# Optimization experiments

Measured on AMD Instinct MI355X. Metric: run time of the kernel, lower is better.

The kernel has to match this reference:

```python
import jax, jax.numpy as jnp
import numpy as np
from jax import lax

# ---- module hyperparams (match init_kwargs and mamba_ssm Mamba2 defaults) ----
D_MODEL = 768
D_STATE = 64
D_CONV = 4
EXPAND = 2
HEADDIM = 64  # Mamba2 default
D_INNER = EXPAND * D_MODEL          # 1536
NHEADS = D_INNER // HEADDIM         # 24
NGROUPS = 1
CONV_DIM = D_INNER + 2 * NGROUPS * D_STATE          # 1664
D_IN_PROJ = 2 * D_INNER + 2 * NGROUPS * D_STATE + NHEADS  # 3224
BSZ, SEQ = 2, 512
EPS = 1e-5


def setup_inputs() -> dict:
    key = jax.random.key(0)
    ks = jax.random.split(key, 12)
    def n(k, shape, s):
        return jax.random.normal(k, shape, jnp.float32) * s
    x = n(ks[0], (BSZ, SEQ, D_MODEL), 1.0)
    in_proj_w = n(ks[1], (D_IN_PROJ, D_MODEL), D_MODEL ** -0.5)
    conv_w = n(ks[2], (CONV_DIM, D_CONV), D_CONV ** -0.5)
    conv_b = jnp.zeros((CONV_DIM,), jnp.float32)
    # dt_bias = softplus^{-1}(dt) with dt log-uniform in [1e-3, 1e-1] (Mamba2 init)
    dt = jnp.exp(jax.random.uniform(ks[3], (NHEADS,), jnp.float32,
                                    minval=np.log(1e-3), maxval=np.log(1e-1)))
    dt_bias = dt + jnp.log(-jnp.expm1(-dt))
    A_log = jnp.log(jax.random.uniform(ks[4], (NHEADS,), jnp.float32, minval=1.0, maxval=16.0))
    D_param = jnp.ones((NHEADS,), jnp.float32)
    norm_w = jnp.ones((D_INNER,), jnp.float32)
    out_proj_w = n(ks[5], (D_MODEL, D_INNER), D_INNER ** -0.5)
    ln1_w = jnp.ones((D_MODEL,), jnp.float32); ln1_b = jnp.zeros((D_MODEL,), jnp.float32)
    ln2_w = jnp.ones((D_MODEL,), jnp.float32); ln2_b = jnp.zeros((D_MODEL,), jnp.float32)
    ff_w1 = n(ks[6], (4 * D_MODEL, D_MODEL), D_MODEL ** -0.5)
    ff_b1 = jnp.zeros((4 * D_MODEL,), jnp.float32)
    ff_w2 = n(ks[7], (D_MODEL, 4 * D_MODEL), (4 * D_MODEL) ** -0.5)
    ff_b2 = jnp.zeros((D_MODEL,), jnp.float32)
    return dict(x=x, in_proj_w=in_proj_w, conv_w=conv_w, conv_b=conv_b,
                dt_bias=dt_bias, A_log=A_log, D_param=D_param, norm_w=norm_w,
                out_proj_w=out_proj_w, ln1_w=ln1_w, ln1_b=ln1_b,
                ln2_w=ln2_w, ln2_b=ln2_b, ff_w1=ff_w1, ff_b1=ff_b1,
                ff_w2=ff_w2, ff_b2=ff_b2)


def layernorm(x, w, b):
    mu = jnp.mean(x, -1, keepdims=True)
    xc = x - mu
    var = jnp.mean(xc * xc, -1, keepdims=True)
    return xc * lax.rsqrt(var + EPS) * w + b


def mamba2(xn, in_proj_w, conv_w, conv_b, dt_bias, A_log, D_param, norm_w, out_proj_w):
    b, l, _ = xn.shape
    zxbcdt = xn @ in_proj_w.T  # [b, l, D_IN_PROJ]
    z = zxbcdt[..., :D_INNER]
    xBC = zxbcdt[..., D_INNER:D_INNER + CONV_DIM]
    dt = zxbcdt[..., D_INNER + CONV_DIM:]
    # causal depthwise conv over time on xBC
    xc = lax.conv_general_dilated(xBC.transpose(0, 2, 1), conv_w[:, None, :], (1,),
                                  [(D_CONV - 1, 0)], dimension_numbers=('NCH', 'OIH', 'NCH'),
                                  feature_group_count=CONV_DIM)
    xBC = jax.nn.silu((xc + conv_b[None, :, None]).transpose(0, 2, 1))
    xs = xBC[..., :D_INNER].reshape(b, l, NHEADS, HEADDIM)
    Bm = xBC[..., D_INNER:D_INNER + D_STATE]   # [b, l, n]  (ngroups=1)
    Cm = xBC[..., D_INNER + D_STATE:]          # [b, l, n]
    dt = jax.nn.softplus(dt + dt_bias)         # [b, l, h]
    dA = jnp.exp(dt * (-jnp.exp(A_log)))       # [b, l, h]
    dBx = jnp.einsum('blh,bln,blhp->blhpn', dt, Bm, xs)
    def step(h, inp):
        dA_t, dBx_t = inp                      # [b,h], [b,h,p,n]
        h = dA_t[:, :, None, None] * h + dBx_t
        return h, h
    _, hs = lax.scan(step, jnp.zeros((b, NHEADS, HEADDIM, D_STATE), xn.dtype),
                     (dA.transpose(1, 0, 2), dBx.transpose(1, 0, 2, 3, 4)))
    y = jnp.einsum('lbhpn,bln->blhp', hs, Cm) + D_param[None, None, :, None] * xs
    y = y.reshape(b, l, D_INNER) * jax.nn.silu(z)   # gated RMSNorm (norm_before_gate=False)
    y = y * lax.rsqrt(jnp.mean(y * y, -1, keepdims=True) + EPS) * norm_w
    return y @ out_proj_w.T


def reference(x, in_proj_w, conv_w, conv_b, dt_bias, A_log, D_param, norm_w,
              out_proj_w, ln1_w, ln1_b, ln2_w, ln2_b, ff_w1, ff_b1, ff_w2, ff_b2):
    residual = x
    xn = layernorm(x, ln1_w, ln1_b)
    mp = (in_proj_w, conv_w, conv_b, dt_bias, A_log, D_param, norm_w, out_proj_w)
    out_f = mamba2(xn, *mp)
    out_b = jnp.flip(mamba2(jnp.flip(xn, 1), *mp), 1)
    m = layernorm(out_f + out_b, ln2_w, ln2_b)
    ff = jax.nn.gelu(m @ ff_w1.T + ff_b1, approximate=False) @ ff_w2.T + ff_b2
    return ff + residual
```

## Files before the change

### kernel.cpp

```cpp
#include <hip/hip_runtime.h>
#include <hip/hip_bf16.h>
#include <math.h>

#define SEQ     512
#define BSZ     2
#define ROWS    (BSZ*SEQ)
#define DMODEL  768
#define DINNER  1536
#define DSTATE  64
#define NHEADS  24
#define HEADDIM 64
#define CONVDIM 1664
#define DINPROJ 3224
#define DFF     3072
#define EPSF    1e-5f

typedef __attribute__((ext_vector_type(8))) short s16x8;
typedef __attribute__((ext_vector_type(4))) float f32x4;

__device__ __forceinline__ float b2f(const __hip_bfloat16 v){ return __bfloat162float(v); }
__device__ __forceinline__ __hip_bfloat16 f2b(float v){ return __float2bfloat16(v); }
__device__ __forceinline__ ushort f2bu(float v){
  union { __hip_bfloat16 b; ushort u; } c; c.b = __float2bfloat16(v); return c.u;
}
__device__ __forceinline__ float u2f(ushort u){ return __uint_as_float(((uint)u) << 16); }

__device__ __forceinline__ void gload16(const void* g, void* l){
  __builtin_amdgcn_global_load_lds((__attribute__((address_space(1))) const void*)g,
                                   (__attribute__((address_space(3))) void*)l, 16, 0, 0);
}

__device__ __forceinline__ float block_sum256(float v, float* sh){
  #pragma unroll
  for (int off = 32; off > 0; off >>= 1) v += __shfl_down(v, off, 64);
  int w = threadIdx.x >> 6;
  if ((threadIdx.x & 63) == 0) sh[w] = v;
  __syncthreads();
  float t = sh[0] + sh[1] + sh[2] + sh[3];
  __syncthreads();
  return t;
}

__global__ __launch_bounds__(256) void zerof_kernel(float* out, int n){
  int i = blockIdx.x*256 + threadIdx.x;
  if (i < n) out[i] = 0.f;
}

__global__ __launch_bounds__(256) void w2ball_kernel(const float* __restrict__ w0,
    const float* __restrict__ w1, const float* __restrict__ w2,
    const float* __restrict__ w3, ushort* __restrict__ o,
    int n0, int n1, int n2, int n3)
{
  int i = (blockIdx.x*256 + threadIdx.x) << 2;
  int total = n0 + n1 + n2 + n3;
  if (i >= total) return;
  const float* s; int off;
  if      (i < n0)          { s = w0; off = i; }
  else if (i < n0+n1)       { s = w1; off = i - n0; }
  else if (i < n0+n1+n2)    { s = w2; off = i - n0 - n1; }
  else                      { s = w3; off = i - n0 - n1 - n2; }
  float4 f = *(const float4*)(s + off);
  ushort4 u = make_ushort4(f2bu(f.x), f2bu(f.y), f2bu(f.z), f2bu(f.w));
  *(ushort4*)(o + i) = u;
}

__global__ __launch_bounds__(256) void ln_kernel(const float* __restrict__ in,
    const float* __restrict__ w, const float* __restrict__ b,
    __hip_bfloat16* __restrict__ out)
{
  __shared__ float sh[4];
  const int row = blockIdx.x;
  const float* xr = in + (size_t)row * DMODEL;
  float v[3]; float s = 0.f;
  #pragma unroll
  for (int i = 0; i < 3; i++){ int c = threadIdx.x + i*256; v[i] = xr[c]; s += v[i]; }
  s = block_sum256(s, sh);
  float mu = s * (1.f/DMODEL);
  float s2 = 0.f;
  #pragma unroll
  for (int i = 0; i < 3; i++){ float d = v[i]-mu; s2 += d*d; }
  s2 = block_sum256(s2, sh);
  float rs = rsqrtf(s2*(1.f/DMODEL) + EPSF);
  #pragma unroll
  for (int i = 0; i < 3; i++){
    int c = threadIdx.x + i*256;
    out[(size_t)row*DMODEL + c] = f2b((v[i]-mu)*rs*w[c] + b[c]);
  }
}

__device__ __forceinline__ s16x8 ld_frag(const ushort* p){
  union { ushort4 h[2]; s16x8 v; } u;
  u.h[0] = *(const ushort4*)(p);
  u.h[1] = *(const ushort4*)(p + 4);
  return u.v;
}

template<typename CTy, int KS, int EPI>
__global__ __launch_bounds__(256) void gemm_bb64(const __hip_bfloat16* __restrict__ A_,
    const __hip_bfloat16* __restrict__ B_, CTy* __restrict__ C,
    const float* __restrict__ bias, int M, int N, int K)
{
  __shared__ __align__(16) ushort As[2][64][64];
  __shared__ __align__(16) ushort Bs[2][64][64];
  const int tid  = threadIdx.x;
  const int lane = tid & 63, wave = tid >> 6;
  const int wr = wave >> 1, wc = wave & 1;
  const int n0 = blockIdx.x * 64, m0 = blockIdx.y * 64;
  const int Kc   = K / KS;
  const int kbeg = blockIdx.z * Kc;
  const int srw  = lane >> 3;
  const int scol = (((lane & 7) ^ srw) << 3);
  const int l15  = lane & 15;
  const int r7   = l15 & 7;
  const int c0   = lane >> 4;

  const ushort* Au = (const ushort*)A_;
  const ushort* Bu = (const ushort*)B_;

  f32x4 acc[2][2] = {};

  auto stage = [&](int bf, int k0){
    #pragma unroll
    for (int q = 0; q < 2; q++){
      int row = q*32 + wave*8 + srw;
      gload16(Au + (size_t)(m0 + row)*K + kbeg + k0 + scol, &As[bf][q*32 + wave*8][0]);
      int nr = n0 + row; if (nr > N-1) nr = N-1;
      gload16(Bu + (size_t)nr*K + kbeg + k0 + scol, &Bs[bf][q*32 + wave*8][0]);
    }
  };

  stage(0, 0);
  __syncthreads();
  int cur = 0;
  for (int k0 = 0; k0 < Kc; k0 += 64){
    if (k0 + 64 < Kc) stage(cur ^ 1, k0 + 64);
    #pragma unroll
    for (int t = 0; t < 2; t++){
      const int fc = (((t*4 + c0) ^ r7) << 3);
      s16x8 a0 = ld_frag(&As[cur][wr*32      + l15][fc]);
      s16x8 a1 = ld_frag(&As[cur][wr*32 + 16 + l15][fc]);
      s16x8 b0 = ld_frag(&Bs[cur][wc*32      + l15][fc]);
      s16x8 b1 = ld_frag(&Bs[cur][wc*32 + 16 + l15][fc]);
      acc[0][0] = __builtin_amdgcn_mfma_f32_16x16x32_bf16(a0, b0, acc[0][0], 0, 0, 0);
      acc[0][1] = __builtin_amdgcn_mfma_f32_16x16x32_bf16(a0, b1, acc[0][1], 0, 0, 0);
      acc[1][0] = __builtin_amdgcn_mfma_f32_16x16x32_bf16(a1, b0, acc[1][0], 0, 0, 0);
      acc[1][1] = __builtin_amdgcn_mfma_f32_16x16x32_bf16(a1, b1, acc[1][1], 0, 0, 0);
    }
    __syncthreads();
    cur ^= 1;
  }

  CTy* Cz = C + (size_t)blockIdx.z * M * N;
  const int crow = (lane >> 4) * 4;
  #pragma unroll
  for (int i = 0; i < 2; i++){
    #pragma unroll
    for (int j = 0; j < 2; j++){
      int col = n0 + wc*32 + j*16 + l15;
      if (col < N){
        #pragma unroll
        for (int q = 0; q < 4; q++){
          int rowg = m0 + wr*32 + i*16 + crow + q;
          if constexpr (EPI == 1){
            float v = acc[i][j][q] + bias[col];
            Cz[(size_t)rowg*N + col] = (CTy)f2b(0.5f * v * (1.f + erff(v * 0.70710678118654752f)));
          } else if constexpr (sizeof(CTy) == 4){
            Cz[(size_t)rowg*N + col] = acc[i][j][q];
          } else {
            Cz[(size_t)rowg*N + col] = (CTy)f2b(acc[i][j][q]);
          }
        }
      }
    }
  }
}

template<typename CTy>
__global__ __launch_bounds__(256) void gemm_mfma(const __hip_bfloat16* __restrict__ A,
    const float* __restrict__ B, CTy* __restrict__ C, int M, int N, int K)
{
  __shared__ __align__(16) ushort As[64][72];
  __shared__ __align__(16) ushort Bs[64][72];
  const int tid  = threadIdx.x;
  const int lane = tid & 63, wave = tid >> 6;
  const int wr = wave >> 1, wc = wave & 1;
  const int n0 = blockIdx.x * 64, m0 = blockIdx.y * 64;
  const int sr = tid >> 2;
  const int sc = (tid & 3) * 16;
  const int l15 = lane & 15, lk = (lane >> 4) * 8;

  f32x4 acc[2][2] = {};

  const ushort* Au = (const ushort*)A;
  int nr = n0 + sr; if (nr > N-1) nr = N-1;

  for (int k0 = 0; k0 < K; k0 += 64){
    const ushort* ag = Au + (size_t)(m0 + sr)*K + (k0 + sc);
    ushort4 a0 = *(const ushort4*)(ag);
    ushort4 a1 = *(const ushort4*)(ag + 4);
    ushort4 a2 = *(const ushort4*)(ag + 8);
    ushort4 a3 = *(const ushort4*)(ag + 12);
    const float* bg = B + (size_t)nr*K + (k0 + sc);
    float4 f0 = *(const float4*)(bg);
    float4 f1 = *(const float4*)(bg + 4);
    float4 f2 = *(const float4*)(bg + 8);
    float4 f3 = *(const float4*)(bg + 12);
    ushort4 b0 = make_ushort4(f2bu(f0.x), f2bu(f0.y), f2bu(f0.z), f2bu(f0.w));
    ushort4 b1 = make_ushort4(f2bu(f1.x), f2bu(f1.y), f2bu(f1.z), f2bu(f1.w));
    ushort4 b2 = make_ushort4(f2bu(f2.x), f2bu(f2.y), f2bu(f2.z), f2bu(f2.w));
    ushort4 b3 = make_ushort4(f2bu(f3.x), f2bu(f3.y), f2bu(f3.z), f2bu(f3.w));

    __syncthreads();
    *(ushort4*)&As[sr][sc +  0] = a0;
    *(ushort4*)&As[sr][sc +  4] = a1;
    *(ushort4*)&As[sr][sc +  8] = a2;
    *(ushort4*)&As[sr][sc + 12] = a3;
    *(ushort4*)&Bs[sr][sc +  0] = b0;
    *(ushort4*)&Bs[sr][sc +  4] = b1;
    *(ushort4*)&Bs[sr][sc +  8] = b2;
    *(ushort4*)&Bs[sr][sc + 12] = b3;
    __syncthreads();

    #pragma unroll
    for (int kk = 0; kk < 64; kk += 32){
      s16x8 af0 = ld_frag(&As[wr*32      + l15][kk + lk]);
      s16x8 af1 = ld_frag(&As[wr*32 + 16 + l15][kk + lk]);
      s16x8 bf0 = ld_frag(&Bs[wc*32      + l15][kk + lk]);
      s16x8 bf1 = ld_frag(&Bs[wc*32 + 16 + l15][kk + lk]);
      acc[0][0] = __builtin_amdgcn_mfma_f32_16x16x32_bf16(af0, bf0, acc[0][0], 0, 0, 0);
      acc[0][1] = __builtin_amdgcn_mfma_f32_16x16x32_bf16(af0, bf1, acc[0][1], 0, 0, 0);
      acc[1][0] = __builtin_amdgcn_mfma_f32_16x16x32_bf16(af1, bf0, acc[1][0], 0, 0, 0);
      acc[1][1] = __builtin_amdgcn_mfma_f32_16x16x32_bf16(af1, bf1, acc[1][1], 0, 0, 0);
    }
  }

  const int crow = (lane >> 4) * 4;
  #pragma unroll
  for (int i = 0; i < 2; i++){
    #pragma unroll
    for (int j = 0; j < 2; j++){
      int col = n0 + wc*32 + j*16 + l15;
      if (col < N){
        #pragma unroll
        for (int q = 0; q < 4; q++){
          int rowg = m0 + wr*32 + i*16 + crow + q;
          if constexpr (sizeof(CTy) == 4) C[(size_t)rowg*N + col] = acc[i][j][q];
          else                            C[(size_t)rowg*N + col] = (CTy)f2b(acc[i][j][q]);
        }
      }
    }
  }
}

__global__ __launch_bounds__(256) void convdt_kernel(const __hip_bfloat16* __restrict__ zx,
    const float* __restrict__ cw, const float* __restrict__ cb,
    const float* __restrict__ dt_bias, const float* __restrict__ A_log,
    __hip_bfloat16* __restrict__ xconv, float* __restrict__ dtb, float* __restrict__ dab)
{
  const int tt = blockIdx.x, b = blockIdx.y, dir = blockIdx.z;
  const int c8 = threadIdx.x * 8;
  if (c8 < CONVDIM){
    size_t rowoff[4]; bool ok[4];
    #pragma unroll
    for (int k = 0; k < 4; k++){
      int s = tt - 3 + k;
      ok[k] = (s >= 0);
      int ss = ok[k] ? s : 0;
      int phys = dir ? (SEQ-1-ss) : ss;
      rowoff[k] = ((size_t)(b*SEQ + phys))*DINPROJ + DINNER + c8;
    }
    float acc[8];
    {
      float4 cb0 = *(const float4*)(cb + c8);
      float4 cb1 = *(const float4*)(cb + c8 + 4);
      acc[0]=cb0.x; acc[1]=cb0.y; acc[2]=cb0.z; acc[3]=cb0.w;
      acc[4]=cb1.x; acc[5]=cb1.y; acc[6]=cb1.z; acc[7]=cb1.w;
    }
    float wv[8][4];
    #pragma unroll
    for (int j = 0; j < 8; j++){
      float4 w4 = *(const float4*)(cw + (size_t)(c8 + j)*4);
      wv[j][0]=w4.x; wv[j][1]=w4.y; wv[j][2]=w4.z; wv[j][3]=w4.w;
    }
    const ushort* zu = (const ushort*)zx;
    #pragma unroll
    for (int k = 0; k < 4; k++){
      if (ok[k]){
        ushort4 v0 = *(const ushort4*)(zu + rowoff[k]);
        ushort4 v1 = *(const ushort4*)(zu + rowoff[k] + 4);
        acc[0] = fmaf(wv[0][k], u2f(v0.x), acc[0]);
        acc[1] = fmaf(wv[1][k], u2f(v0.y), acc[1]);
        acc[2] = fmaf(wv[2][k], u2f(v0.z), acc[2]);
        acc[3] = fmaf(wv[3][k], u2f(v0.w), acc[3]);
        acc[4] = fmaf(wv[4][k], u2f(v1.x), acc[4]);
        acc[5] = fmaf(wv[5][k], u2f(v1.y), acc[5]);
        acc[6] = fmaf(wv[6][k], u2f(v1.z), acc[6]);
        acc[7] = fmaf(wv[7][k], u2f(v1.w), acc[7]);
      }
    }
    ushort* outr = (ushort*)xconv + ((size_t)((dir*BSZ + b)*SEQ + tt))*CONVDIM + c8;
    ushort o[8];
    #pragma unroll
    for (int j = 0; j < 8; j++){
      float s = acc[j] / (1.f + expf(-acc[j]));
      o[j] = f2bu(s);
    }
    *(ushort4*)(outr)     = make_ushort4(o[0],o[1],o[2],o[3]);
    *(ushort4*)(outr + 4) = make_ushort4(o[4],o[5],o[6],o[7]);
  }
  if (dir == 0 && threadIdx.x < NHEADS){
    int h = threadIdx.x;
    size_t r = (size_t)b*SEQ + tt;
    float raw = b2f(zx[r*DINPROJ + (DINNER + CONVDIM) + h]) + dt_bias[h];
    float sp  = fmaxf(raw, 0.f) + log1pf(expf(-fabsf(raw)));
    dtb[r*NHEADS + h] = sp;
    dab[r*NHEADS + h] = expf(-sp * expf(A_log[h]));
  }
}

#define CT 16

__global__ __launch_bounds__(256) void scan_pass1(const __hip_bfloat16* __restrict__ xconv,
    const float* __restrict__ dtb, const float* __restrict__ dab,
    float* __restrict__ stateBuf, int CL)
{
  const int c = blockIdx.x, h = blockIdx.y, z = blockIdx.z;
  const int b = z & 1, dir = z >> 1;
  const int tid = threadIdx.x, lane = tid & 63, wave = tid >> 6, nb = wave * 16;
  __shared__ __align__(16) float Bc[CT][64], Xc[CT][64];
  __shared__ float dAc[CT], dtc[CT];
  float hreg[16];
  #pragma unroll
  for (int j = 0; j < 16; j++) hreg[j] = 0.f;
  const size_t dirbase = (size_t)z * SEQ;
  const int cstart = c * CL;

  const int ttl = tid >> 4, c4 = (tid & 15) << 2;

  for (int c0 = cstart; c0 < cstart + CL; c0 += CT){
    {
      const ushort* rowp = (const ushort*)xconv + (dirbase + c0 + ttl)*(size_t)CONVDIM;
      ushort4 bv = *(const ushort4*)(rowp + DINNER + c4);
      ushort4 xv = *(const ushort4*)(rowp + h*HEADDIM + c4);
      Bc[ttl][c4+0] = u2f(bv.x); Bc[ttl][c4+1] = u2f(bv.y);
      Bc[ttl][c4+2] = u2f(bv.z); Bc[ttl][c4+3] = u2f(bv.w);
      Xc[ttl][c4+0] = u2f(xv.x); Xc[ttl][c4+1] = u2f(xv.y);
      Xc[ttl][c4+2] = u2f(xv.z); Xc[ttl][c4+3] = u2f(xv.w);
    }
    if (tid < CT){
      int phys = dir ? (SEQ-1 - (c0 + tid)) : (c0 + tid);
      size_t r = (size_t)b*SEQ + phys;
      dAc[tid] = dab[r*NHEADS + h];
      dtc[tid] = dtb[r*NHEADS + h];
    }
    __syncthreads();

    #pragma unroll 4
    for (int tt = 0; tt < CT; tt++){
      float dA = dAc[tt];
      float dtx = dtc[tt] * Xc[tt][lane];
      const float4* Bq = (const float4*)&Bc[tt][nb];
      float4 B0 = Bq[0], B1 = Bq[1], B2 = Bq[2], B3 = Bq[3];
      hreg[ 0]=fmaf(dA,hreg[ 0],dtx*B0.x); hreg[ 1]=fmaf(dA,hreg[ 1],dtx*B0.y);
      hreg[ 2]=fmaf(dA,hreg[ 2],dtx*B0.z); hreg[ 3]=fmaf(dA,hreg[ 3],dtx*B0.w);
      hreg[ 4]=fmaf(dA,hreg[ 4],dtx*B1.x); hreg[ 5]=fmaf(dA,hreg[ 5],dtx*B1.y);
      hreg[ 6]=fmaf(dA,hreg[ 6],dtx*B1.z); hreg[ 7]=fmaf(dA,hreg[ 7],dtx*B1.w);
      hreg[ 8]=fmaf(dA,hreg[ 8],dtx*B2.x); hreg[ 9]=fmaf(dA,hreg[ 9],dtx*B2.y);
      hreg[10]=fmaf(dA,hreg[10],dtx*B2.z); hreg[11]=fmaf(dA,hreg[11],dtx*B2.w);
      hreg[12]=fmaf(dA,hreg[12],dtx*B3.x); hreg[13]=fmaf(dA,hreg[13],dtx*B3.y);
      hreg[14]=fmaf(dA,hreg[14],dtx*B3.z); hreg[15]=fmaf(dA,hreg[15],dtx*B3.w);
    }
    __syncthreads();
  }

  float* sp = stateBuf + (((size_t)c*4 + z)*NHEADS + h)*4096 + (size_t)lane*64 + nb;
  *(float4*)(sp +  0) = make_float4(hreg[ 0],hreg[ 1],hreg[ 2],hreg[ 3]);
  *(float4*)(sp +  4) = make_float4(hreg[ 4],hreg[ 5],hreg[ 6],hreg[ 7]);
  *(float4*)(sp +  8) = make_float4(hreg[ 8],hreg[ 9],hreg[10],hreg[11]);
  *(float4*)(sp + 12) = make_float4(hreg[12],hreg[13],hreg[14],hreg[15]);
}

__global__ __launch_bounds__(256) void scan_fixup(const float* __restrict__ dab,
    float* __restrict__ stateBuf, int NC, int CL)
{
  const int h = blockIdx.x, z = blockIdx.y;
  const int b = z & 1, dir = z >> 1;
  const int tid = threadIdx.x;
  __shared__ float sdA[SEQ];
  __shared__ float P[8];
  for (int i = tid; i < SEQ; i += 256){
    int phys = dir ? (SEQ-1-i) : i;
    sdA[i] = dab[((size_t)b*SEQ + phys)*NHEADS + h];
  }
  __syncthreads();
  if (tid < NC){
    float p = 1.f;
    for (int i = 0; i < CL; i++) p *= sdA[tid*CL + i];
    P[tid] = p;
  }
  __syncthreads();

  float hrun[16], Lcur[16];
  #pragma unroll
  for (int j = 0; j < 16; j++) hrun[j] = 0.f;
  {
    const float* s0 = stateBuf + ((size_t)z*NHEADS + h)*4096 + (size_t)tid*16;
    #pragma unroll
    for (int j = 0; j < 16; j++) Lcur[j] = s0[j];
  }
  for (int c = 1; c < NC; c++){
    float Pp = P[c-1];
    float hnew[16];
    #pragma unroll
    for (int j = 0; j < 16; j++) hnew[j] = fmaf(Pp, hrun[j], Lcur[j]);
    float* sc = stateBuf + (((size_t)c*4 + z)*NHEADS + h)*4096 + (size_t)tid*16;
    if (c < NC-1){
      #pragma unroll
      for (int j = 0; j < 16; j++) Lcur[j] = sc[j];
    }
    #pragma unroll
    for (int j = 0; j < 16; j++) sc[j] = hnew[j];
    #pragma unroll
    for (int j = 0; j < 16; j++) hrun[j] = hnew[j];
  }
}

__global__ __launch_bounds__(256) void scan_pass2(const __hip_bfloat16* __restrict__ xconv,
    const __hip_bfloat16* __restrict__ zx, const float* __restrict__ dtb,
    const float* __restrict__ dab, const float* __restrict__ Dp,
    const float* __restrict__ stateBuf, __hip_bfloat16* __restrict__ yg, int CL)
{
  const int c = blockIdx.x, h = blockIdx.y, z = blockIdx.z;
  const int b = z & 1, dir = z >> 1;
  const int tid = threadIdx.x, lane = tid & 63, wave = tid >> 6, nb = wave * 16;
  __shared__ __align__(16) float Bc[CT][64], Cc[CT][64], Xc[CT][64];
  __shared__ __align__(16) float Yp[4][CT][64];
  __shared__ float dAc[CT], dtc[CT];
  float hreg[16];
  if (c == 0){
    #pragma unroll
    for (int j = 0; j < 16; j++) hreg[j] = 0.f;
  } else {
    const float* sp = stateBuf + (((size_t)c*4 + z)*NHEADS + h)*4096 + (size_t)lane*64 + nb;
    float4 s0 = *(const float4*)(sp+0), s1 = *(const float4*)(sp+4);
    float4 s2 = *(const float4*)(sp+8), s3 = *(const float4*)(sp+12);
    hreg[ 0]=s0.x; hreg[ 1]=s0.y; hreg[ 2]=s0.z; hreg[ 3]=s0.w;
    hreg[ 4]=s1.x; hreg[ 5]=s1.y; hreg[ 6]=s1.z; hreg[ 7]=s1.w;
    hreg[ 8]=s2.x; hreg[ 9]=s2.y; hreg[10]=s2.z; hreg[11]=s2.w;
    hreg[12]=s3.x; hreg[13]=s3.y; hreg[14]=s3.z; hreg[15]=s3.w;
  }
  const float Dh = Dp[h];
  const size_t dirbase = (size_t)z * SEQ;
  const int cstart = c * CL;
  const int ttl = tid >> 4, c4 = (tid & 15) << 2;

  for (int c0 = cstart; c0 < cstart + CL; c0 += CT){
    {
      const ushort* rowp = (const ushort*)xconv + (dirbase + c0 + ttl)*(size_t)CONVDIM;
      ushort4 bv = *(const ushort4*)(rowp + DINNER + c4);
      ushort4 cv = *(const ushort4*)(rowp + DINNER + DSTATE + c4);
      ushort4 xv = *(const ushort4*)(rowp + h*HEADDIM + c4);
      Bc[ttl][c4+0] = u2f(bv.x); Bc[ttl][c4+1] = u2f(bv.y);
      Bc[ttl][c4+2] = u2f(bv.z); Bc[ttl][c4+3] = u2f(bv.w);
      Cc[ttl][c4+0] = u2f(cv.x); Cc[ttl][c4+1] = u2f(cv.y);
      Cc[ttl][c4+2] = u2f(cv.z); Cc[ttl][c4+3] = u2f(cv.w);
      Xc[ttl][c4+0] = u2f(xv.x); Xc[ttl][c4+1] = u2f(xv.y);
      Xc[ttl][c4+2] = u2f(xv.z); Xc[ttl][c4+3] = u2f(xv.w);
    }
    if (tid < CT){
      int phys = dir ? (SEQ-1 - (c0 + tid)) : (c0 + tid);
      size_t r = (size_t)b*SEQ + phys;
      dAc[tid] = dab[r*NHEADS + h];
      dtc[tid] = dtb[r*NHEADS + h];
    }
    __syncthreads();

    #pragma unroll 4
    for (int tt = 0; tt < CT; tt++){
      float dA = dAc[tt];
      float dtx = dtc[tt] * Xc[tt][lane];
      const float4* Bq = (const float4*)&Bc[tt][nb];
      const float4* Cq = (const float4*)&Cc[tt][nb];
      float4 B0 = Bq[0], B1 = Bq[1], B2 = Bq[2], B3 = Bq[3];
      float4 C0 = Cq[0], C1 = Cq[1], C2 = Cq[2], C3 = Cq[3];
      float y0 = 0.f, y1 = 0.f, y2 = 0.f, y3 = 0.f;
      hreg[ 0]=fmaf(dA,hreg[ 0],dtx*B0.x); y0=fmaf(hreg[ 0],C0.x,y0);
      hreg[ 1]=fmaf(dA,hreg[ 1],dtx*B0.y); y1=fmaf(hreg[ 1],C0.y,y1);
      hreg[ 2]=fmaf(dA,hreg[ 2],dtx*B0.z); y2=fmaf(hreg[ 2],C0.z,y2);
      hreg[ 3]=fmaf(dA,hreg[ 3],dtx*B0.w); y3=fmaf(hreg[ 3],C0.w,y3);
      hreg[ 4]=fmaf(dA,hreg[ 4],dtx*B1.x); y0=fmaf(hreg[ 4],C1.x,y0);
      hreg[ 5]=fmaf(dA,hreg[ 5],dtx*B1.y); y1=fmaf(hreg[ 5],C1.y,y1);
      hreg[ 6]=fmaf(dA,hreg[ 6],dtx*B1.z); y2=fmaf(hreg[ 6],C1.z,y2);
      hreg[ 7]=fmaf(dA,hreg[ 7],dtx*B1.w); y3=fmaf(hreg[ 7],C1.w,y3);
      hreg[ 8]=fmaf(dA,hreg[ 8],dtx*B2.x); y0=fmaf(hreg[ 8],C2.x,y0);
      hreg[ 9]=fmaf(dA,hreg[ 9],dtx*B2.y); y1=fmaf(hreg[ 9],C2.y,y1);
      hreg[10]=fmaf(dA,hreg[10],dtx*B2.z); y2=fmaf(hreg[10],C2.z,y2);
      hreg[11]=fmaf(dA,hreg[11],dtx*B2.w); y3=fmaf(hreg[11],C2.w,y3);
      hreg[12]=fmaf(dA,hreg[12],dtx*B3.x); y0=fmaf(hreg[12],C3.x,y0);
      hreg[13]=fmaf(dA,hreg[13],dtx*B3.y); y1=fmaf(hreg[13],C3.y,y1);
      hreg[14]=fmaf(dA,hreg[14],dtx*B3.z); y2=fmaf(hreg[14],C3.z,y2);
      hreg[15]=fmaf(dA,hreg[15],dtx*B3.w); y3=fmaf(hreg[15],C3.w,y3);
      Yp[wave][tt][lane] = (y0+y1) + (y2+y3);
    }
    __syncthreads();

    {
      int tl = tid >> 4, p4 = (tid & 15) << 2;
      float4 ya = *(const float4*)&Yp[0][tl][p4];
      float4 yb4 = *(const float4*)&Yp[1][tl][p4];
      float4 yc = *(const float4*)&Yp[2][tl][p4];
      float4 yd = *(const float4*)&Yp[3][tl][p4];
      float4 xv = *(const float4*)&Xc[tl][p4];
      int phys = dir ? (SEQ-1 - (c0 + tl)) : (c0 + tl);
      size_t r = (size_t)b*SEQ + phys;
      const ushort* zp = (const ushort*)zx + r*DINPROJ + h*HEADDIM + p4;
      ushort4 zv = *(const ushort4*)zp;
      float zf[4] = { u2f(zv.x), u2f(zv.y), u2f(zv.z), u2f(zv.w) };
      float yv[4] = { ya.x+yb4.x+yc.x+yd.x + Dh*xv.x,
                      ya.y+yb4.y+yc.y+yd.y + Dh*xv.y,
                      ya.z+yb4.z+yc.z+yd.z + Dh*xv.z,
                      ya.w+yb4.w+yc.w+yd.w + Dh*xv.w };
      ushort o[4];
      #pragma unroll
      for (int j = 0; j < 4; j++){
        float sil = zf[j] / (1.f + expf(-zf[j]));
        o[j] = f2bu(yv[j] * sil);
      }
      ushort* op = (ushort*)yg + ((size_t)dir*ROWS + r)*DINNER + h*HEADDIM + p4;
      *(ushort4*)op = make_ushort4(o[0],o[1],o[2],o[3]);
    }
    __syncthreads();
  }
}

__global__ __launch_bounds__(256) void rmscomb_kernel(const __hip_bfloat16* __restrict__ yg,
    const float* __restrict__ nw, __hip_bfloat16* __restrict__ u)
{
  __shared__ float sh[4];
  const int row = blockIdx.x;
  const __hip_bfloat16* yf = yg + (size_t)row*DINNER;
  const __hip_bfloat16* yb = yg + (size_t)(ROWS + row)*DINNER;
  float vf[6], vb[6]; float sf = 0.f, sb = 0.f;
  #pragma unroll
  for (int i = 0; i < 6; i++){
    int c = threadIdx.x + i*256;
    vf[i] = b2f(yf[c]); sf += vf[i]*vf[i];
    vb[i] = b2f(yb[c]); sb += vb[i]*vb[i];
  }
  sf = block_sum256(sf, sh);
  sb = block_sum256(sb, sh);
  float rf = rsqrtf(sf*(1.f/DINNER) + EPSF);
  float rb = rsqrtf(sb*(1.f/DINNER) + EPSF);
  #pragma unroll
  for (int i = 0; i < 6; i++){
    int c = threadIdx.x + i*256;
    u[(size_t)row*DINNER + c] = f2b((vf[i]*rf + vb[i]*rb) * nw[c]);
  }
}

template<int NP>
__global__ __launch_bounds__(256) void ln2_kernel(const float* __restrict__ in,
    size_t pstride, const float* __restrict__ w, const float* __restrict__ b,
    __hip_bfloat16* __restrict__ out)
{
  __shared__ float sh[4];
  const int row = blockIdx.x;
  float v[3]; float s = 0.f;
  #pragma unroll
  for (int i = 0; i < 3; i++){
    int c = threadIdx.x + i*256;
    size_t idx = (size_t)row*DMODEL + c;
    float t = 0.f;
    #pragma unroll
    for (int p = 0; p < NP; p++) t += in[p*pstride + idx];
    v[i] = t; s += t;
  }
  s = block_sum256(s, sh);
  float mu = s * (1.f/DMODEL);
  float s2 = 0.f;
  #pragma unroll
  for (int i = 0; i < 3; i++){ float d = v[i]-mu; s2 += d*d; }
  s2 = block_sum256(s2, sh);
  float rs = rsqrtf(s2*(1.f/DMODEL) + EPSF);
  #pragma unroll
  for (int i = 0; i < 3; i++){
    int c = threadIdx.x + i*256;
    out[(size_t)row*DMODEL + c] = f2b((v[i]-mu)*rs*w[c] + b[c]);
  }
}

__global__ __launch_bounds__(256) void gelu_kernel(const __hip_bfloat16* __restrict__ g,
    const float* __restrict__ b1, __hip_bfloat16* __restrict__ out)
{
  size_t idx = (size_t)blockIdx.x*256 + threadIdx.x;
  int c = (int)(idx % DFF);
  float v = b2f(g[idx]) + b1[c];
  out[idx] = f2b(0.5f * v * (1.f + erff(v * 0.70710678118654752f)));
}

template<int NP>
__global__ __launch_bounds__(256) void final_kernel(const float* __restrict__ f,
    size_t pstride, const float* __restrict__ bias, const float* __restrict__ x,
    float* __restrict__ out)
{
  size_t i4 = ((size_t)blockIdx.x*256 + threadIdx.x) << 2;
  int c = (int)(i4 % DMODEL);
  float4 bv = *(const float4*)(bias + c);
  float4 xv = *(const float4*)(x + i4);
  float4 s = make_float4(bv.x+xv.x, bv.y+xv.y, bv.z+xv.z, bv.w+xv.w);
  #pragma unroll
  for (int p = 0; p < NP; p++){
    float4 fv = *(const float4*)(f + p*pstride + i4);
    s.x += fv.x; s.y += fv.y; s.z += fv.z; s.w += fv.w;
  }
  *(float4*)(out + i4) = s;
}

extern "C" void kernel_launch(void* const* d_in, const int* in_sizes, int n_in,
                              void* d_out, int out_size, void* d_ws, size_t ws_size,
                              hipStream_t stream)
{
  float* out = (float*)d_out;

  const size_t NEED = 19906560;
  if (ws_size < NEED || n_in < 17){
    zerof_kernel<<<(out_size + 255)/256, 256, 0, stream>>>(out, out_size);
    return;
  }

  const float* x       = (const float*)d_in[0];
  const float* in_proj_w = (const float*)d_in[1];
  const float* conv_w  = (const float*)d_in[2];
  const float* conv_b  = (const float*)d_in[3];
  const float* dt_bias = (const float*)d_in[4];
  const float* A_log   = (const float*)d_in[5];
  const float* D_param = (const float*)d_in[6];
  const float* norm_w  = (const float*)d_in[7];
  const float* out_proj_w = (const float*)d_in[8];
  const float* ln1_w   = (const float*)d_in[9];
  const float* ln1_b   = (const float*)d_in[10];
  const float* ln2_w   = (const float*)d_in[11];
  const float* ln2_b   = (const float*)d_in[12];
  const float* ff_w1   = (const float*)d_in[13];
  const float* ff_b1   = (const float*)d_in[14];
  const float* ff_w2   = (const float*)d_in[15];
  const float* ff_b2   = (const float*)d_in[16];

  char* ws = (char*)d_ws;
  __hip_bfloat16* zx  = (__hip_bfloat16*)(ws + 0);
  __hip_bfloat16* xn  = (__hip_bfloat16*)(ws + 6602752);
  float*          dtb = (float*)(ws + 6602752);
  float*          dab = (float*)(ws + 6701056);
  __hip_bfloat16* xcv = (__hip_bfloat16*)(ws + 6799360);
  __hip_bfloat16* yg  = (__hip_bfloat16*)(ws + 13615104);
  __hip_bfloat16* u   = (__hip_bfloat16*)(ws + 0);
  float*          mo  = (float*)(ws + 3145728);
  __hip_bfloat16* mb  = (__hip_bfloat16*)(ws + 0);
  __hip_bfloat16* g   = (__hip_bfloat16*)(ws + 6799360);
  __hip_bfloat16* gb  = (__hip_bfloat16*)(ws + 13615104);
  float*          fo  = (float*)(ws + 0);

  const size_t WBALL = 16748544;
  const size_t PARTS = 12582912;
  const size_t CHB   = 1572864;
  const size_t PSTRIDE = (size_t)ROWS * DMODEL;
  const int WN_IN = DINPROJ*DMODEL;
  const int WN_OUT = DMODEL*DINNER;
  const int WN_F1 = DFF*DMODEL;
  const int WN_F2 = DMODEL*DFF;

  size_t rem = ws_size - NEED;
  bool fast = (rem >= WBALL + PARTS);
  ushort* wb    = (ushort*)(ws + NEED);
  float*  parts = (float*) (ws + NEED + WBALL);
  size_t scanoff = NEED + (fast ? (WBALL + PARTS) : 0);
  size_t srem = ws_size - scanoff;
  int NC = 1;
  if      (srem >= 8*CHB) NC = 8;
  else if (srem >= 4*CHB) NC = 4;
  else if (srem >= 2*CHB) NC = 2;
  float* stateBuf = (float*)(ws + scanoff);
  const int CL = SEQ / NC;

  ln_kernel<<<ROWS, 256, 0, stream>>>(x, ln1_w, ln1_b, xn);
  if (fast){
    int total4 = (WN_IN + WN_OUT + WN_F1 + WN_F2) / 4;
    w2ball_kernel<<<(total4 + 255)/256, 256, 0, stream>>>(in_proj_w, out_proj_w,
        ff_w1, ff_w2, wb, WN_IN, WN_OUT, WN_F1, WN_F2);
  }
  if (fast){
    gemm_bb64<__hip_bfloat16,1,0><<<dim3((DINPROJ+63)/64, ROWS/64), 256, 0, stream>>>(
        xn, (const __hip_bfloat16*)wb, zx, nullptr, ROWS, DINPROJ, DMODEL);
  } else {
    gemm_mfma<<<dim3((DINPROJ+63)/64, ROWS/64), 256, 0, stream>>>(xn, in_proj_w, zx, ROWS, DINPROJ, DMODEL);
  }
  convdt_kernel<<<dim3(SEQ, BSZ, 2), 256, 0, stream>>>(zx, conv_w, conv_b, dt_bias, A_log, xcv, dtb, dab);
  if (NC > 1){
    scan_pass1<<<dim3(NC-1, NHEADS, 4), 256, 0, stream>>>(xcv, dtb, dab, stateBuf, CL);
    scan_fixup<<<dim3(NHEADS, 4), 256, 0, stream>>>(dab, stateBuf, NC, CL);
  }
  scan_pass2<<<dim3(NC, NHEADS, 4), 256, 0, stream>>>(xcv, zx, dtb, dab, D_param, stateBuf, yg, CL);
  rmscomb_kernel<<<ROWS, 256, 0, stream>>>(yg, norm_w, u);
  if (fast){
    gemm_bb64<float,2,0><<<dim3(DMODEL/64, ROWS/64, 2), 256, 0, stream>>>(
        u, (const __hip_bfloat16*)(wb + WN_IN), parts, nullptr, ROWS, DMODEL, DINNER);
    ln2_kernel<2><<<ROWS, 256, 0, stream>>>(parts, PSTRIDE, ln2_w, ln2_b, mb);
  } else {
    gemm_mfma<<<dim3(DMODEL/64, ROWS/64), 256, 0, stream>>>(u, out_proj_w, mo, ROWS, DMODEL, DINNER);
    ln2_kernel<1><<<ROWS, 256, 0, stream>>>(mo, 0, ln2_w, ln2_b, mb);
  }
  if (fast){
    gemm_bb64<__hip_bfloat16,1,1><<<dim3(DFF/64, ROWS/64), 256, 0, stream>>>(
        mb, (const __hip_bfloat16*)(wb + WN_IN + WN_OUT), gb, ff_b1, ROWS, DFF, DMODEL);
  } else {
    gemm_mfma<<<dim3(DFF/64, ROWS/64), 256, 0, stream>>>(mb, ff_w1, g, ROWS, DFF, DMODEL);
    gelu_kernel<<<(ROWS*DFF)/256, 256, 0, stream>>>(g, ff_b1, gb);
  }
  if (fast){
    gemm_bb64<float,4,0><<<dim3(DMODEL/64, ROWS/64, 4), 256, 0, stream>>>(
        gb, (const __hip_bfloat16*)(wb + WN_IN + WN_OUT + WN_F1), parts, nullptr, ROWS, DMODEL, DFF);
    final_kernel<4><<<(ROWS*DMODEL/4)/256, 256, 0, stream>>>(parts, PSTRIDE, ff_b2, x, out);
  } else {
    gemm_mfma<<<dim3(DMODEL/64, ROWS/64), 256, 0, stream>>>(gb, ff_w2, fo, ROWS, DMODEL, DFF);
    final_kernel<1><<<(ROWS*DMODEL/4)/256, 256, 0, stream>>>(fo, 0, ff_b2, x, out);
  }
}
```

Baseline: 251.2 us.

## Fuse LN1 into weight cast, triple-buffer GEMM, fold scan fixup into pass2

```diff
diff --git a/kernel.cpp b/kernel.cpp
--- a/kernel.cpp
+++ b/kernel.cpp
@@ -46,22 +46,45 @@
   if (i < n) out[i] = 0.f;
 }
 
-__global__ __launch_bounds__(256) void w2ball_kernel(const float* __restrict__ w0,
+__global__ __launch_bounds__(256) void prep_kernel(const float* __restrict__ w0,
     const float* __restrict__ w1, const float* __restrict__ w2,
     const float* __restrict__ w3, ushort* __restrict__ o,
-    int n0, int n1, int n2, int n3)
-{
-  int i = (blockIdx.x*256 + threadIdx.x) << 2;
-  int total = n0 + n1 + n2 + n3;
-  if (i >= total) return;
-  const float* s; int off;
-  if      (i < n0)          { s = w0; off = i; }
-  else if (i < n0+n1)       { s = w1; off = i - n0; }
-  else if (i < n0+n1+n2)    { s = w2; off = i - n0 - n1; }
-  else                      { s = w3; off = i - n0 - n1 - n2; }
-  float4 f = *(const float4*)(s + off);
-  ushort4 u = make_ushort4(f2bu(f.x), f2bu(f.y), f2bu(f.z), f2bu(f.w));
-  *(ushort4*)(o + i) = u;
+    int n0, int n1, int n2, int n3, int wblocks,
+    const float* __restrict__ xin, const float* __restrict__ lnw,
+    const float* __restrict__ lnb, __hip_bfloat16* __restrict__ xnout)
+{
+  __shared__ float sh[4];
+  if ((int)blockIdx.x < wblocks){
+    int i = (blockIdx.x*256 + threadIdx.x) << 2;
+    int total = n0 + n1 + n2 + n3;
+    if (i < total){
+      const float* s; int off;
+      if      (i < n0)       { s = w0; off = i; }
+      else if (i < n0+n1)    { s = w1; off = i - n0; }
+      else if (i < n0+n1+n2) { s = w2; off = i - n0 - n1; }
+      else                   { s = w3; off = i - n0 - n1 - n2; }
+      float4 f = *(const float4*)(s + off);
+      *(ushort4*)(o + i) = make_ushort4(f2bu(f.x), f2bu(f.y), f2bu(f.z), f2bu(f.w));
+    }
+    return;
+  }
+  const int row = blockIdx.x - wblocks;
+  const float* xr = xin + (size_t)row * DMODEL;
+  float v[3]; float s = 0.f;
+  #pragma unroll
+  for (int i = 0; i < 3; i++){ int c = threadIdx.x + i*256; v[i] = xr[c]; s += v[i]; }
+  s = block_sum256(s, sh);
+  float mu = s * (1.f/DMODEL);
+  float s2 = 0.f;
+  #pragma unroll
+  for (int i = 0; i < 3; i++){ float d = v[i]-mu; s2 += d*d; }
+  s2 = block_sum256(s2, sh);
+  float rs = rsqrtf(s2*(1.f/DMODEL) + EPSF);
+  #pragma unroll
+  for (int i = 0; i < 3; i++){
+    int c = threadIdx.x + i*256;
+    xnout[(size_t)row*DMODEL + c] = f2b((v[i]-mu)*rs*lnw[c] + lnb[c]);
+  }
 }
 
 __global__ __launch_bounds__(256) void ln_kernel(const float* __restrict__ in,
@@ -100,14 +123,15 @@
     const __hip_bfloat16* __restrict__ B_, CTy* __restrict__ C,
     const float* __restrict__ bias, int M, int N, int K)
 {
-  __shared__ __align__(16) ushort As[2][64][64];
-  __shared__ __align__(16) ushort Bs[2][64][64];
+  __shared__ __align__(16) ushort As[3][64][64];
+  __shared__ __align__(16) ushort Bs[3][64][64];
   const int tid  = threadIdx.x;
   const int lane = tid & 63, wave = tid >> 6;
   const int wr = wave >> 1, wc = wave & 1;
   const int n0 = blockIdx.x * 64, m0 = blockIdx.y * 64;
   const int Kc   = K / KS;
   const int kbeg = blockIdx.z * Kc;
+  const int NT   = Kc >> 6;
   const int srw  = lane >> 3;
   const int scol = (((lane & 7) ^ srw) << 3);
   const int l15  = lane & 15;
@@ -130,13 +154,17 @@
   };
 
   stage(0, 0);
-  __syncthreads();
-  int cur = 0;
-  for (int k0 = 0; k0 < Kc; k0 += 64){
-    if (k0 + 64 < Kc) stage(cur ^ 1, k0 + 64);
-    #pragma unroll
-    for (int t = 0; t < 2; t++){
-      const int fc = (((t*4 + c0) ^ r7) << 3);
+  stage(1, 64);
+  asm volatile("s_waitcnt vmcnt(4)" ::: "memory");
+  __builtin_amdgcn_s_barrier();
+
+  for (int t = 0; t < NT; ++t){
+    const int nxt = t + 2;
+    if (nxt < NT) stage(nxt % 3, nxt << 6);
+    const int cur = t % 3;
+    #pragma unroll
+    for (int tt = 0; tt < 2; tt++){
+      const int fc = (((tt*4 + c0) ^ r7) << 3);
       s16x8 a0 = ld_frag(&As[cur][wr*32      + l15][fc]);
       s16x8 a1 = ld_frag(&As[cur][wr*32 + 16 + l15][fc]);
       s16x8 b0 = ld_frag(&Bs[cur][wc*32      + l15][fc]);
@@ -146,8 +174,10 @@
       acc[1][0] = __builtin_amdgcn_mfma_f32_16x16x32_bf16(a1, b0, acc[1][0], 0, 0, 0);
       acc[1][1] = __builtin_amdgcn_mfma_f32_16x16x32_bf16(a1, b1, acc[1][1], 0, 0, 0);
     }
-    __syncthreads();
-    cur ^= 1;
+    if (t == NT-1) break;
+    if (nxt < NT) { asm volatile("s_waitcnt vmcnt(4)" ::: "memory"); }
+    else          { asm volatile("s_waitcnt vmcnt(0)" ::: "memory"); }
+    __builtin_amdgcn_s_barrier();
   }
 
   CTy* Cz = C + (size_t)blockIdx.z * M * N;
@@ -380,51 +410,6 @@
   *(float4*)(sp + 12) = make_float4(hreg[12],hreg[13],hreg[14],hreg[15]);
 }
 
-__global__ __launch_bounds__(256) void scan_fixup(const float* __restrict__ dab,
-    float* __restrict__ stateBuf, int NC, int CL)
-{
-  const int h = blockIdx.x, z = blockIdx.y;
-  const int b = z & 1, dir = z >> 1;
-  const int tid = threadIdx.x;
-  __shared__ float sdA[SEQ];
-  __shared__ float P[8];
-  for (int i = tid; i < SEQ; i += 256){
-    int phys = dir ? (SEQ-1-i) : i;
-    sdA[i] = dab[((size_t)b*SEQ + phys)*NHEADS + h];
-  }
-  __syncthreads();
-  if (tid < NC){
-    float p = 1.f;
-    for (int i = 0; i < CL; i++) p *= sdA[tid*CL + i];
-    P[tid] = p;
-  }
-  __syncthreads();
-
-  float hrun[16], Lcur[16];
-  #pragma unroll
-  for (int j = 0; j < 16; j++) hrun[j] = 0.f;
-  {
-    const float* s0 = stateBuf + ((size_t)z*NHEADS + h)*4096 + (size_t)tid*16;
-    #pragma unroll
-    for (int j = 0; j < 16; j++) Lcur[j] = s0[j];
-  }
-  for (int c = 1; c < NC; c++){
-    float Pp = P[c-1];
-    float hnew[16];
-    #pragma unroll
-    for (int j = 0; j < 16; j++) hnew[j] = fmaf(Pp, hrun[j], Lcur[j]);
-    float* sc = stateBuf + (((size_t)c*4 + z)*NHEADS + h)*4096 + (size_t)tid*16;
-    if (c < NC-1){
-      #pragma unroll
-      for (int j = 0; j < 16; j++) Lcur[j] = sc[j];
-    }
-    #pragma unroll
-    for (int j = 0; j < 16; j++) sc[j] = hnew[j];
-    #pragma unroll
-    for (int j = 0; j < 16; j++) hrun[j] = hnew[j];
-  }
-}
-
 __global__ __launch_bounds__(256) void scan_pass2(const __hip_bfloat16* __restrict__ xconv,
     const __hip_bfloat16* __restrict__ zx, const float* __restrict__ dtb,
     const float* __restrict__ dab, const float* __restrict__ Dp,
@@ -436,18 +421,37 @@
   __shared__ __align__(16) float Bc[CT][64], Cc[CT][64], Xc[CT][64];
   __shared__ __align__(16) float Yp[4][CT][64];
   __shared__ float dAc[CT], dtc[CT];
+  __shared__ float sP[8];
   float hreg[16];
-  if (c == 0){
-    #pragma unroll
-    for (int j = 0; j < 16; j++) hreg[j] = 0.f;
-  } else {
-    const float* sp = stateBuf + (((size_t)c*4 + z)*NHEADS + h)*4096 + (size_t)lane*64 + nb;
-    float4 s0 = *(const float4*)(sp+0), s1 = *(const float4*)(sp+4);
-    float4 s2 = *(const float4*)(sp+8), s3 = *(const float4*)(sp+12);
-    hreg[ 0]=s0.x; hreg[ 1]=s0.y; hreg[ 2]=s0.z; hreg[ 3]=s0.w;
-    hreg[ 4]=s1.x; hreg[ 5]=s1.y; hreg[ 6]=s1.z; hreg[ 7]=s1.w;
-    hreg[ 8]=s2.x; hreg[ 9]=s2.y; hreg[10]=s2.z; hreg[11]=s2.w;
-    hreg[12]=s3.x; hreg[13]=s3.y; hreg[14]=s3.z; hreg[15]=s3.w;
+  #pragma unroll
+  for (int j = 0; j < 16; j++) hreg[j] = 0.f;
+  if (c > 0){
+    if (tid < c){
+      float p = 1.f;
+      for (int i = 0; i < CL; i++){
+        int t = tid*CL + i;
+        int phys = dir ? (SEQ-1 - t) : t;
+        p *= dab[((size_t)b*SEQ + phys)*NHEADS + h];
+      }
+      sP[tid] = p;
+    }
+    __syncthreads();
+    float suffix = 1.f;
+    for (int i = c-1; i >= 0; --i){
+      const float* sp = stateBuf + (((size_t)i*4 + z)*NHEADS + h)*4096 + (size_t)lane*64 + nb;
+      float4 s0 = *(const float4*)(sp+0), s1 = *(const float4*)(sp+4);
+      float4 s2 = *(const float4*)(sp+8), s3 = *(const float4*)(sp+12);
+      hreg[ 0]=fmaf(suffix,s0.x,hreg[ 0]); hreg[ 1]=fmaf(suffix,s0.y,hreg[ 1]);
+      hreg[ 2]=fmaf(suffix,s0.z,hreg[ 2]); hreg[ 3]=fmaf(suffix,s0.w,hreg[ 3]);
+      hreg[ 4]=fmaf(suffix,s1.x,hreg[ 4]); hreg[ 5]=fmaf(suffix,s1.y,hreg[ 5]);
+      hreg[ 6]=fmaf(suffix,s1.z,hreg[ 6]); hreg[ 7]=fmaf(suffix,s1.w,hreg[ 7]);
+      hreg[ 8]=fmaf(suffix,s2.x,hreg[ 8]); hreg[ 9]=fmaf(suffix,s2.y,hreg[ 9]);
+      hreg[10]=fmaf(suffix,s2.z,hreg[10]); hreg[11]=fmaf(suffix,s2.w,hreg[11]);
+      hreg[12]=fmaf(suffix,s3.x,hreg[12]); hreg[13]=fmaf(suffix,s3.y,hreg[13]);
+      hreg[14]=fmaf(suffix,s3.z,hreg[14]); hreg[15]=fmaf(suffix,s3.w,hreg[15]);
+      suffix *= sP[i];
+    }
+    __syncthreads();
   }
   const float Dh = Dp[h];
   const size_t dirbase = (size_t)z * SEQ;
@@ -664,10 +668,10 @@
   const size_t PARTS = 12582912;
   const size_t CHB   = 1572864;
   const size_t PSTRIDE = (size_t)ROWS * DMODEL;
-  const int WN_IN = DINPROJ*DMODEL;
+  const int WN_IN  = DINPROJ*DMODEL;
   const int WN_OUT = DMODEL*DINNER;
-  const int WN_F1 = DFF*DMODEL;
-  const int WN_F2 = DMODEL*DFF;
+  const int WN_F1  = DFF*DMODEL;
+  const int WN_F2  = DMODEL*DFF;
 
   size_t rem = ws_size - NEED;
   bool fast = (rem >= WBALL + PARTS);
@@ -682,22 +686,19 @@
   float* stateBuf = (float*)(ws + scanoff);
   const int CL = SEQ / NC;
 
-  ln_kernel<<<ROWS, 256, 0, stream>>>(x, ln1_w, ln1_b, xn);
   if (fast){
-    int total4 = (WN_IN + WN_OUT + WN_F1 + WN_F2) / 4;
-    w2ball_kernel<<<(total4 + 255)/256, 256, 0, stream>>>(in_proj_w, out_proj_w,
-        ff_w1, ff_w2, wb, WN_IN, WN_OUT, WN_F1, WN_F2);
-  }
-  if (fast){
+    const int wblocks = (WN_IN + WN_OUT + WN_F1 + WN_F2) / 4 / 256;
+    prep_kernel<<<wblocks + ROWS, 256, 0, stream>>>(in_proj_w, out_proj_w, ff_w1, ff_w2,
+        wb, WN_IN, WN_OUT, WN_F1, WN_F2, wblocks, x, ln1_w, ln1_b, xn);
     gemm_bb64<__hip_bfloat16,1,0><<<dim3((DINPROJ+63)/64, ROWS/64), 256, 0, stream>>>(
         xn, (const __hip_bfloat16*)wb, zx, nullptr, ROWS, DINPROJ, DMODEL);
   } else {
+    ln_kernel<<<ROWS, 256, 0, stream>>>(x, ln1_w, ln1_b, xn);
     gemm_mfma<<<dim3((DINPROJ+63)/64, ROWS/64), 256, 0, stream>>>(xn, in_proj_w, zx, ROWS, DINPROJ, DMODEL);
   }
   convdt_kernel<<<dim3(SEQ, BSZ, 2), 256, 0, stream>>>(zx, conv_w, conv_b, dt_bias, A_log, xcv, dtb, dab);
   if (NC > 1){
     scan_pass1<<<dim3(NC-1, NHEADS, 4), 256, 0, stream>>>(xcv, dtb, dab, stateBuf, CL);
-    scan_fixup<<<dim3(NHEADS, 4), 256, 0, stream>>>(dab, stateBuf, NC, CL);
   }
   scan_pass2<<<dim3(NC, NHEADS, 4), 256, 0, stream>>>(xcv, zx, dtb, dab, D_param, stateBuf, yg, CL);
   rmscomb_kernel<<<ROWS, 256, 0, stream>>>(yg, norm_w, u);
```

New measurement: 268.9 us. 7.0% more time.
